# Performance work log

Hardware: AMD Instinct MI355X
Metric: run time of the kernel (lower is better)

Reference implementation:

```python
import jax, jax.numpy as jnp
import numpy as np

B, T, NX, H = 2, 2048, 1024, 16
D = NX // H  # head dim = 64
NEG = -1e9


def setup_inputs() -> dict:
    key = jax.random.key(0)
    ks = jax.random.split(key, 4)
    std = 0.02
    x = jax.random.normal(ks[0], (B, T, NX), dtype=jnp.float32)
    # non-trivial adjacency (lower-triangular) so the masking branch is active
    adj = jnp.tril(jnp.ones((T, T), dtype=jnp.float32))
    w_attn = jax.random.normal(ks[1], (NX, 3 * NX), dtype=jnp.float32) * std
    b_attn = jnp.zeros((3 * NX,), dtype=jnp.float32)
    w_proj = jax.random.normal(ks[2], (NX, NX), dtype=jnp.float32) * std
    b_proj = jnp.zeros((NX,), dtype=jnp.float32)
    w_proj1 = jax.random.normal(ks[3], (NX, NX), dtype=jnp.float32) * std
    b_proj1 = jnp.zeros((NX,), dtype=jnp.float32)
    return {"x": x, "adj": adj, "w_attn": w_attn, "b_attn": b_attn,
            "w_proj": w_proj, "b_proj": b_proj,
            "w_proj1": w_proj1, "b_proj1": b_proj1}


def reference(x, adj, w_attn, b_attn, w_proj, b_proj, w_proj1, b_proj1):
    # c_attn: fused qkv projection  [B,T,3*NX]
    qkv = jnp.einsum('btn,nm->btm', x, w_attn) + b_attn
    q, k, v = jnp.split(qkv, 3, axis=-1)  # each [B,T,NX]

    def heads(t):  # [B,T,NX] -> [B,H,T,D]
        return t.reshape(B, T, H, D).transpose(0, 2, 1, 3)

    qh, kh, vh = heads(q), heads(k), heads(v)
    # scale=False in module default: raw dot-product scores
    w = jnp.einsum('bhqd,bhkd->bhqk', qh, kh)  # [B,H,T,T]
    w = w * adj + NEG * (1.0 - adj)            # custom adjacency mask
    w = jax.nn.softmax(w, axis=-1)
    a = jnp.einsum('bhqk,bhkd->bhqd', w, vh)   # [B,H,T,D]
    a = a.transpose(0, 2, 1, 3).reshape(B, T, NX)  # merge heads
    a = jnp.einsum('btn,nm->btm', a, w_proj) + b_proj
    # residue branch: split+merge of query is identity -> c_proj_1(q)
    re = jnp.einsum('btn,nm->btm', q, w_proj1) + b_proj1
    return a + re
```

## Files before the change

### kernel.cpp

```cpp
#include <hip/hip_runtime.h>
#include <stdint.h>

typedef short s16x8 __attribute__((ext_vector_type(8)));
typedef float f32x4 __attribute__((ext_vector_type(4)));
typedef unsigned int u32x4 __attribute__((ext_vector_type(4)));

#define AS1 __attribute__((address_space(1)))
#define AS3 __attribute__((address_space(3)))

static constexpr int Bc = 2, Tc = 2048, NXc = 1024, Hc = 16;
static constexpr float NEGC = -1e9f;
static constexpr float L2E = 1.44269504088896340736f;
static constexpr float LN2 = 0.69314718055994530942f;

static __device__ __forceinline__ unsigned short f2bf(float f) {
  uint32_t u = __builtin_bit_cast(uint32_t, f);
  u += 0x7fffu + ((u >> 16) & 1u);
  return (unsigned short)(u >> 16);
}

static __device__ __forceinline__ float exp2fast(float x) {
  return __builtin_amdgcn_exp2f(x);
}

static __device__ __forceinline__ uint32_t cvt_pk_bf16(float lo, float hi) {
  uint32_t r;
  asm("v_cvt_pk_bf16_f32 %0, %1, %2" : "=v"(r) : "v"(lo), "v"(hi));
  return r;
}

static __device__ __forceinline__ void gload_lds16(const void* g, void* l) {
  __builtin_amdgcn_global_load_lds((const AS1 uint32_t*)g, (AS3 uint32_t*)l, 16, 0, 0);
}

__global__ __launch_bounds__(256) void k_prep(
    const float* __restrict__ x, unsigned short* __restrict__ xb,
    const float* __restrict__ w_attn, unsigned short* __restrict__ wattnT,
    const float* __restrict__ w_proj, const float* __restrict__ w_proj1,
    unsigned short* __restrict__ wcatT,
    const float* __restrict__ adj, unsigned char* __restrict__ tm) {
  __shared__ float tile[32][33];
  __shared__ int s_any, s_all;
  const int bid = blockIdx.x;
  const int t = threadIdx.x;

  if (bid < 4096) {
    int i = bid * 256 + t;
    float4 v = ((const float4*)x)[i];
    uint32_t lo = (uint32_t)f2bf(v.x) | ((uint32_t)f2bf(v.y) << 16);
    uint32_t hi = (uint32_t)f2bf(v.z) | ((uint32_t)f2bf(v.w) << 16);
    ((uint2*)xb)[i] = make_uint2(lo, hi);
    return;
  }
  if (bid < 9216) {
    const float* src; unsigned short* dst;
    int scols, dld, dkoff, n0, k0; float scale;
    if (bid < 7168) {
      int b = bid - 4096; n0 = (b % 96) * 32; k0 = (b / 96) * 32;
      src = w_attn; scols = 3072; dst = wattnT; dld = 1024; dkoff = 0; scale = 1.0f;
    } else if (bid < 8192) {
      int b = bid - 7168; n0 = (b & 31) * 32; k0 = (b >> 5) * 32;
      src = w_proj; scols = 1024; dst = wcatT; dld = 2048; dkoff = 0; scale = 1.0f;
    } else {
      int b = bid - 8192; n0 = (b & 31) * 32; k0 = (b >> 5) * 32;
      src = w_proj1; scols = 1024; dst = wcatT; dld = 2048; dkoff = 1024; scale = LN2;
    }
    int tx = t & 31, ty = t >> 5;
#pragma unroll
    for (int r = 0; r < 4; r++)
      tile[ty + r * 8][tx] = src[(size_t)(k0 + ty + r * 8) * scols + n0 + tx];
    __syncthreads();
#pragma unroll
    for (int r = 0; r < 4; r++) {
      int n = n0 + ty + r * 8;
      dst[(size_t)n * dld + dkoff + k0 + tx] = f2bf(tile[tx][ty + r * 8] * scale);
    }
    return;
  }
  {
    int b = bid - 9216;
    int kt = b & 31, qt = b >> 5;
    bool anyv = false, all1 = true;
#pragma unroll
    for (int i = 0; i < 4; i++) {
      int e = t * 4 + i;
      int row = e >> 4, c4 = e & 15;
      float4 v = *(const float4*)&adj[(size_t)(qt * 64 + row) * Tc + kt * 64 + c4 * 4];
      anyv |= (v.x != 0.f) | (v.y != 0.f) | (v.z != 0.f) | (v.w != 0.f);
      all1 &= (v.x == 1.f) & (v.y == 1.f) & (v.z == 1.f) & (v.w == 1.f);
    }
    if (t == 0) { s_any = 0; s_all = 1; }
    __syncthreads();
    if (anyv) s_any = 1;
    if (!all1) s_all = 0;
    __syncthreads();
    if (t == 0) tm[qt * 32 + kt] = (unsigned char)(s_any ? (s_all ? 2 : 1) : 0);
  }
}

__global__ __launch_bounds__(256) void k_gemm0(
    const unsigned short* __restrict__ A, int lda,
    const unsigned short* __restrict__ BT, int K,
    const float* __restrict__ bias0, unsigned short* __restrict__ Cb) {
  __shared__ __align__(16) unsigned short As[128 * 32];
  __shared__ __align__(16) unsigned short Bs[128 * 32];
  const int nbx = gridDim.x, nby = gridDim.y;
  const int nwg = nbx * nby;
  int id = blockIdx.y * nbx + blockIdx.x;
  id = (id & 7) * (nwg >> 3) + (id >> 3);
  const int bx = id % nbx;
  const int by = id / nbx;
  const int m0 = by * 128;
  const int n0 = bx * 128;

  const int lane = threadIdx.x & 63;
  const int w = threadIdx.x >> 6;
  const int wr = (w >> 1) * 64;
  const int wc = (w & 1) * 64;
  const int g = lane >> 4, lr = lane & 15;
  const int srow = lane >> 2;
  const int scol = lane & 3;
  f32x4 acc[4][4] = {};

  for (int k0 = 0; k0 < K; k0 += 32) {
    __syncthreads();
#pragma unroll
    for (int i = 0; i < 2; i++) {
      int c = w * 2 + i;
      int row = c * 16 + srow;
      int cs = scol ^ (row & 3);
      gload_lds16(A + (size_t)(m0 + row) * lda + k0 + cs * 8, (void*)(As + c * 512));
      gload_lds16(BT + (size_t)(n0 + row) * K + k0 + cs * 8, (void*)(Bs + c * 512));
    }
    __syncthreads();
    s16x8 af[4], bfr[4];
#pragma unroll
    for (int m = 0; m < 4; m++) {
      int row = wr + m * 16 + lr;
      af[m] = *(const s16x8*)((const char*)As + row * 64 + ((g ^ (row & 3)) * 16));
    }
#pragma unroll
    for (int n = 0; n < 4; n++) {
      int row = wc + n * 16 + lr;
      bfr[n] = *(const s16x8*)((const char*)Bs + row * 64 + ((g ^ (row & 3)) * 16));
    }
#pragma unroll
    for (int m = 0; m < 4; m++)
#pragma unroll
      for (int n = 0; n < 4; n++)
        acc[m][n] = __builtin_amdgcn_mfma_f32_16x16x32_bf16(af[m], bfr[n], acc[m][n], 0, 0, 0);
  }

#pragma unroll
  for (int m = 0; m < 4; m++) {
    int row = m0 + wr + m * 16 + g * 4;
#pragma unroll
    for (int n = 0; n < 4; n++) {
      int col = n0 + wc + n * 16 + lr;
      float bs = bias0[col];
      float sc = (col < NXc) ? L2E : 1.0f;
#pragma unroll
      for (int jj = 0; jj < 4; jj++)
        Cb[(size_t)(row + jj) * 3072 + col] = f2bf((acc[m][n][jj] + bs) * sc);
    }
  }
}

__global__ __launch_bounds__(256) void k_gemm1(
    const unsigned short* __restrict__ A, int lda,
    const unsigned short* __restrict__ A2, int lda2,
    const unsigned short* __restrict__ BT,
    const float* __restrict__ bias0, const float* __restrict__ bias1,
    float* __restrict__ Cf) {
  constexpr int K = 2048, ksplit = 1024;
  __shared__ __align__(16) unsigned short As[2][64 * 32];
  __shared__ __align__(16) unsigned short Bs[2][128 * 32];
  const int nbx = gridDim.x, nby = gridDim.y;
  const int nwg = nbx * nby;
  int id = blockIdx.y * nbx + blockIdx.x;
  id = (id & 7) * (nwg >> 3) + (id >> 3);
  const int bx = id % nbx;
  const int by = id / nbx;
  const int m0 = by * 64;
  const int n0 = bx * 128;

  const int tid = threadIdx.x;
  const int lane = tid & 63;
  const int w = tid >> 6;
  const int wr = (w >> 1) * 32;
  const int wc = (w & 1) * 64;
  const int g = lane >> 4, lr = lane & 15;
  const int srow = lane >> 2;
  const int scol = lane & 3;
  const int arow = tid >> 2;
  f32x4 acc[2][4] = {};

  auto stage = [&](int k0, int buf) {
    {
      int acs = (tid & 3) ^ (arow & 3);
      const unsigned short* ap = (k0 < ksplit)
          ? A + (size_t)(m0 + arow) * lda + k0
          : A2 + (size_t)(m0 + arow) * lda2 + (k0 - ksplit);
      gload_lds16(ap + acs * 8, (void*)(&As[buf][0] + w * 512));
    }
#pragma unroll
    for (int i = 0; i < 2; i++) {
      int c = w * 2 + i;
      int row = c * 16 + srow;
      int cs = scol ^ (row & 3);
      gload_lds16(BT + (size_t)(n0 + row) * K + k0 + cs * 8, (void*)(&Bs[buf][0] + c * 512));
    }
  };

  stage(0, 0);
  __syncthreads();

  for (int k0 = 0; k0 < K; k0 += 32) {
    const int cur = (k0 >> 5) & 1;
    if (k0 + 32 < K) stage(k0 + 32, cur ^ 1);
    s16x8 af[2], bfr[4];
#pragma unroll
    for (int m = 0; m < 2; m++) {
      int row = wr + m * 16 + lr;
      af[m] = *(const s16x8*)((const char*)&As[cur][0] + row * 64 + ((g ^ (row & 3)) * 16));
    }
#pragma unroll
    for (int n = 0; n < 4; n++) {
      int row = wc + n * 16 + lr;
      bfr[n] = *(const s16x8*)((const char*)&Bs[cur][0] + row * 64 + ((g ^ (row & 3)) * 16));
    }
#pragma unroll
    for (int m = 0; m < 2; m++)
#pragma unroll
      for (int n = 0; n < 4; n++)
        acc[m][n] = __builtin_amdgcn_mfma_f32_16x16x32_bf16(af[m], bfr[n], acc[m][n], 0, 0, 0);
    __syncthreads();
  }

#pragma unroll
  for (int m = 0; m < 2; m++) {
    int row = m0 + wr + m * 16 + g * 4;
#pragma unroll
    for (int n = 0; n < 4; n++) {
      int col = n0 + wc + n * 16 + lr;
      float bs = bias0[col] + bias1[col];
#pragma unroll
      for (int jj = 0; jj < 4; jj++)
        Cf[(size_t)(row + jj) * NXc + col] = acc[m][n][jj] + bs;
    }
  }
}

__global__ __launch_bounds__(256) void k_attn(
    const unsigned short* __restrict__ qkv,
    const float* __restrict__ adj,
    const unsigned char* __restrict__ tm,
    unsigned short* __restrict__ acat) {
  __shared__ __align__(16) unsigned short Kb[2][64 * 64];
  __shared__ __align__(16) unsigned short Vt[2][64 * 72];
  __shared__ int s_kts[33];
  __shared__ unsigned char s_tmv[32];
  __shared__ int s_nkt;

  const int bid = blockIdx.x;
  const int qt = 31 - (bid >> 5);
  const int bh = bid & 31;
  const int h = bh & 15;
  const int b = bh >> 4;
  const int q0 = qt * 64;
  const int tid = threadIdx.x;
  const int lane = tid & 63;
  const int w = tid >> 6;
  const int g = lane >> 4, lr = lane & 15;
  const int sc = tid & 7;
  const int sr = tid >> 3;
  const int kvp = 2 * sr;
  const int prp = (kvp & 32) | (((kvp >> 4) & 1) << 2) | ((kvp & 12) << 1) | (kvp & 3);

  if (w == 0) {
    int kt = lane & 31;
    unsigned char v = tm[qt * 32 + kt];
    bool act = (lane < 32) && (v != 0);
    unsigned long long mk = __ballot(act);
    int n = __popcll(mk);
    if (act) {
      int idx = __popcll(mk & ((1ull << lane) - 1));
      s_kts[idx] = kt;
      s_tmv[idx] = v;
      if (idx == n - 1) s_kts[n] = kt;
    }
    if (lane == 0) s_nkt = n;
  }

  s16x8 qf0, qf1;
  {
    size_t base = (size_t)(b * Tc + q0 + w * 16 + lr) * 3072 + h * 64 + g * 8;
    qf0 = *(const s16x8*)(qkv + base);
    qf1 = *(const s16x8*)(qkv + base + 32);
  }
  f32x4 o[4] = {};
  float lrow = 0.f;

  __syncthreads();
  const int nkt = s_nkt;
  if (nkt == 0) return;

  const unsigned short* kbase = qkv + (size_t)(b * Tc) * 3072 + 1024 + h * 64;
  const unsigned short* vbase = kbase + 1024;

  {
    int kt0 = s_kts[0];
    const unsigned short* kb = kbase + (size_t)kt0 * 64 * 3072;
    gload_lds16(kb + (size_t)sr * 3072 + (sc ^ (sr & 7)) * 8, (void*)(&Kb[0][0] + w * 512));
    gload_lds16(kb + (size_t)(sr + 32) * 3072 + (sc ^ (sr & 7)) * 8,
                (void*)(&Kb[0][0] + 2048 + w * 512));
    const unsigned short* vb = vbase + (size_t)kt0 * 64 * 3072;
    s16x8 v0 = *(const s16x8*)(vb + (size_t)kvp * 3072 + sc * 8);
    s16x8 v1 = *(const s16x8*)(vb + (size_t)(kvp + 1) * 3072 + sc * 8);
    char* vt = (char*)&Vt[0][0];
    int pcol = ((prp + sc * 8) & 63) * 2;
#pragma unroll
    for (int j = 0; j < 8; j++) {
      int d = sc * 8 + j;
      uint32_t pk = (uint32_t)(unsigned short)v0[j] |
                    ((uint32_t)(unsigned short)v1[j] << 16);
      *(uint32_t*)(vt + d * 144 + pcol) = pk;
    }
  }
  __syncthreads();

  for (int i = 0; i < nkt; i++) {
    const int cur = i & 1;
    const int kt = s_kts[i];
    const int tmv = s_tmv[i];
    const int kv0 = kt * 64;
    const int nxt = s_kts[i + 1];

    {
      const unsigned short* kb = kbase + (size_t)nxt * 64 * 3072;
      gload_lds16(kb + (size_t)sr * 3072 + (sc ^ (sr & 7)) * 8,
                  (void*)(&Kb[cur ^ 1][0] + w * 512));
      gload_lds16(kb + (size_t)(sr + 32) * 3072 + (sc ^ (sr & 7)) * 8,
                  (void*)(&Kb[cur ^ 1][0] + 2048 + w * 512));
    }
    const unsigned short* vb = vbase + (size_t)nxt * 64 * 3072;
    s16x8 v0 = *(const s16x8*)(vb + (size_t)kvp * 3072 + sc * 8);
    s16x8 v1 = *(const s16x8*)(vb + (size_t)(kvp + 1) * 3072 + sc * 8);

    f32x4 s[4];
    __builtin_amdgcn_s_setprio(1);
#pragma unroll
    for (int n = 0; n < 4; n++) {
      int kvr = n * 16 + lr;
      const char* kr = (const char*)&Kb[cur][0] + kvr * 128;
      s16x8 a0 = *(const s16x8*)(kr + ((g ^ (kvr & 7)) * 16));
      s16x8 a1 = *(const s16x8*)(kr + (((4 + g) ^ (kvr & 7)) * 16));
      f32x4 z = {};
      z = __builtin_amdgcn_mfma_f32_16x16x32_bf16(a0, qf0, z, 0, 0, 0);
      s[n] = __builtin_amdgcn_mfma_f32_16x16x32_bf16(a1, qf1, z, 0, 0, 0);
    }
    __builtin_amdgcn_s_setprio(0);

    if (tmv != 2) {
      const float* arow = adj + (size_t)(q0 + w * 16 + lr) * Tc + kv0;
#pragma unroll
      for (int n = 0; n < 4; n++) {
        float4 a = *(const float4*)(arow + n * 16 + 4 * g);
        s[n][0] = a.x * s[n][0] + NEGC * (1.0f - a.x);
        s[n][1] = a.y * s[n][1] + NEGC * (1.0f - a.y);
        s[n][2] = a.z * s[n][2] + NEGC * (1.0f - a.z);
        s[n][3] = a.w * s[n][3] + NEGC * (1.0f - a.w);
      }
    }

    float ps0 = 0.f, ps1 = 0.f;
#pragma unroll
    for (int n = 0; n < 4; n++) {
      float p0 = exp2fast(s[n][0]), p1 = exp2fast(s[n][1]);
      float p2 = exp2fast(s[n][2]), p3 = exp2fast(s[n][3]);
      s[n][0] = p0; s[n][1] = p1; s[n][2] = p2; s[n][3] = p3;
      ps0 += (p0 + p1); ps1 += (p2 + p3);
    }
    float ps = ps0 + ps1;
    ps += __shfl_xor(ps, 16);
    ps += __shfl_xor(ps, 32);
    lrow += ps;

    u32x4 pw0, pw1;
    pw0.x = cvt_pk_bf16(s[0][0], s[0][1]);
    pw0.y = cvt_pk_bf16(s[0][2], s[0][3]);
    pw0.z = cvt_pk_bf16(s[1][0], s[1][1]);
    pw0.w = cvt_pk_bf16(s[1][2], s[1][3]);
    pw1.x = cvt_pk_bf16(s[2][0], s[2][1]);
    pw1.y = cvt_pk_bf16(s[2][2], s[2][3]);
    pw1.z = cvt_pk_bf16(s[3][0], s[3][1]);
    pw1.w = cvt_pk_bf16(s[3][2], s[3][3]);
    s16x8 pa0 = __builtin_bit_cast(s16x8, pw0);
    s16x8 pa1 = __builtin_bit_cast(s16x8, pw1);

    __builtin_amdgcn_s_setprio(1);
#pragma unroll
    for (int nd = 0; nd < 4; nd++) {
      int d = nd * 16 + lr;
      const char* vrow = (const char*)&Vt[cur][0] + d * 144;
      int swz = (d >> 3) * 8;
      s16x8 vb0 = *(const s16x8*)(vrow + (((8 * g + swz) & 63) * 2));
      s16x8 vb1 = *(const s16x8*)(vrow + (((32 + 8 * g + swz) & 63) * 2));
      o[nd] = __builtin_amdgcn_mfma_f32_16x16x32_bf16(pa0, vb0, o[nd], 0, 0, 0);
      o[nd] = __builtin_amdgcn_mfma_f32_16x16x32_bf16(pa1, vb1, o[nd], 0, 0, 0);
    }
    __builtin_amdgcn_s_setprio(0);

    {
      char* vt = (char*)&Vt[cur ^ 1][0];
      int pcol = ((prp + sc * 8) & 63) * 2;
#pragma unroll
      for (int j = 0; j < 8; j++) {
        int d = sc * 8 + j;
        uint32_t pk = (uint32_t)(unsigned short)v0[j] |
                      ((uint32_t)(unsigned short)v1[j] << 16);
        *(uint32_t*)(vt + d * 144 + pcol) = pk;
      }
    }
    __syncthreads();
  }

  float inv = lrow > 0.f ? 1.0f / lrow : 0.f;
#pragma unroll
  for (int jj = 0; jj < 4; jj++) {
    float iv = __shfl(inv, 4 * g + jj);
    size_t m = (size_t)(b * Tc + q0 + w * 16 + g * 4 + jj);
#pragma unroll
    for (int nd = 0; nd < 4; nd++)
      acat[m * 1024 + h * 64 + nd * 16 + lr] = f2bf(o[nd][jj] * iv);
  }
}

extern "C" void kernel_launch(void* const* d_in, const int* in_sizes, int n_in,
                              void* d_out, int out_size, void* d_ws, size_t ws_size,
                              hipStream_t stream) {
  const float* x       = (const float*)d_in[0];
  const float* adj     = (const float*)d_in[1];
  const float* w_attn  = (const float*)d_in[2];
  const float* b_attn  = (const float*)d_in[3];
  const float* w_proj  = (const float*)d_in[4];
  const float* b_proj  = (const float*)d_in[5];
  const float* w_proj1 = (const float*)d_in[6];
  const float* b_proj1 = (const float*)d_in[7];
  float* out = (float*)d_out;

  char* ws = (char*)d_ws;
  size_t off = 0;
  unsigned short* xb     = (unsigned short*)(ws + off); off += (size_t)4096 * 1024 * 2;
  unsigned short* wattnT = (unsigned short*)(ws + off); off += (size_t)3072 * 1024 * 2;
  unsigned short* wcatT  = (unsigned short*)(ws + off); off += (size_t)1024 * 2048 * 2;
  unsigned short* qkv    = (unsigned short*)(ws + off); off += (size_t)4096 * 3072 * 2;
  unsigned short* acat   = (unsigned short*)(ws + off); off += (size_t)4096 * 1024 * 2;
  unsigned char*  tmask  = (unsigned char*)(ws + off);  off += 1024;
  (void)ws_size; (void)in_sizes; (void)n_in; (void)out_size;

  k_prep<<<10240, 256, 0, stream>>>(x, xb, w_attn, wattnT, w_proj, w_proj1, wcatT,
                                    adj, tmask);
  k_gemm0<<<dim3(24, 32), 256, 0, stream>>>(xb, 1024, wattnT, 1024, b_attn, qkv);
  k_attn<<<1024, 256, 0, stream>>>(qkv, adj, tmask, acat);
  k_gemm1<<<dim3(8, 64), 256, 0, stream>>>(acat, 1024, qkv, 3072,
                                           wcatT, b_proj, b_proj1, out);
}
```

Before: 130.2 us.

## Balance causal attention work by pairing query tiles and splitting KV across blocks

Each attention block now pairs a high query tile with its mirrored low tile. The high tile's KV range is split into two halves: one block handles the first 17 tiles, and the other handles the rest plus the whole low tile. Partial unnormalized outputs and row sums for the upper half of the sequence go to fp32 slabs, and a new combine kernel merges them into acat. The goal is equal work per block so the causal triangle no longer leaves long-tail blocks. The cost is an extra kernel launch and extra fp32 slab traffic.

```diff
diff --git a/kernel.cpp b/kernel.cpp
--- a/kernel.cpp
+++ b/kernel.cpp
@@ -255,19 +255,21 @@
     const unsigned short* __restrict__ qkv,
     const float* __restrict__ adj,
     const unsigned char* __restrict__ tm,
-    unsigned short* __restrict__ acat) {
+    unsigned short* __restrict__ acat,
+    float* __restrict__ o_slab,
+    float* __restrict__ l_slab) {
   __shared__ __align__(16) unsigned short Kb[2][64 * 64];
   __shared__ __align__(16) unsigned short Vt[2][64 * 72];
-  __shared__ int s_kts[33];
-  __shared__ unsigned char s_tmv[32];
-  __shared__ int s_nkt;
+  __shared__ int s_hi[32], s_lo[32];
+  __shared__ int s_nh, s_nl;
 
   const int bid = blockIdx.x;
-  const int qt = 31 - (bid >> 5);
-  const int bh = bid & 31;
+  const int half = bid & 1;
+  const int bh = (bid >> 1) & 31;
+  const int p = bid >> 6;
+  const int qt_hi = 31 - p, qt_lo = p;
   const int h = bh & 15;
   const int b = bh >> 4;
-  const int q0 = qt * 64;
   const int tid = threadIdx.x;
   const int lane = tid & 63;
   const int w = tid >> 6;
@@ -277,7 +279,9 @@
   const int kvp = 2 * sr;
   const int prp = (kvp & 32) | (((kvp >> 4) & 1) << 2) | ((kvp & 12) << 1) | (kvp & 3);
 
-  if (w == 0) {
+  if (w < 2) {
+    int qt = (w == 0) ? qt_hi : qt_lo;
+    int* dst = (w == 0) ? s_hi : s_lo;
     int kt = lane & 31;
     unsigned char v = tm[qt * 32 + kt];
     bool act = (lane < 32) && (v != 0);
@@ -285,134 +289,61 @@
     int n = __popcll(mk);
     if (act) {
       int idx = __popcll(mk & ((1ull << lane) - 1));
-      s_kts[idx] = kt;
-      s_tmv[idx] = v;
-      if (idx == n - 1) s_kts[n] = kt;
-    }
-    if (lane == 0) s_nkt = n;
-  }
+      dst[idx] = kt | ((int)v << 8);
+    }
+    if (lane == 0) { if (w == 0) s_nh = n; else s_nl = n; }
+  }
+  __syncthreads();
+  const int nh = s_nh, nl = s_nl;
+  const int nA = min(nh, 17);
+  const int nhB = nh - nA;
+  const int nit = (half == 0) ? nA : (nhB + nl);
+
+  auto item_at = [&](int i) -> int {
+    if (half == 0) return s_hi[min(i, nA - 1)];
+    if (i < nhB) return s_hi[nA + i];
+    return s_lo[min(i - nhB, nl - 1)];
+  };
+
+  const unsigned short* kbase = qkv + (size_t)(b * Tc) * 3072 + 1024 + h * 64;
+  const unsigned short* vbase = kbase + 1024;
+
+  f32x4 o[4] = {};
+  float lrow = 0.f;
+  bool switched = (half == 1) && (nhB == 0);
+  int cur_q0 = (half == 0 || nhB > 0) ? qt_hi * 64 : qt_lo * 64;
+
+  auto write_partial = [&]() {
+    size_t rbase = (size_t)(half * 2 + b) * 1024 + (qt_hi * 64 - 1024) + w * 16;
+#pragma unroll
+    for (int jj = 0; jj < 4; jj++) {
+      size_t r = rbase + g * 4 + jj;
+#pragma unroll
+      for (int nd = 0; nd < 4; nd++)
+        o_slab[r * 1024 + h * 64 + nd * 16 + lr] = o[nd][jj];
+    }
+    if (g == 0) l_slab[(rbase + lr) * 16 + h] = lrow;
+  };
 
   s16x8 qf0, qf1;
   {
-    size_t base = (size_t)(b * Tc + q0 + w * 16 + lr) * 3072 + h * 64 + g * 8;
+    size_t base = (size_t)(b * Tc + cur_q0 + w * 16 + lr) * 3072 + h * 64 + g * 8;
     qf0 = *(const s16x8*)(qkv + base);
     qf1 = *(const s16x8*)(qkv + base + 32);
   }
-  f32x4 o[4] = {};
-  float lrow = 0.f;
-
-  __syncthreads();
-  const int nkt = s_nkt;
-  if (nkt == 0) return;
-
-  const unsigned short* kbase = qkv + (size_t)(b * Tc) * 3072 + 1024 + h * 64;
-  const unsigned short* vbase = kbase + 1024;
-
-  {
-    int kt0 = s_kts[0];
-    const unsigned short* kb = kbase + (size_t)kt0 * 64 * 3072;
-    gload_lds16(kb + (size_t)sr * 3072 + (sc ^ (sr & 7)) * 8, (void*)(&Kb[0][0] + w * 512));
-    gload_lds16(kb + (size_t)(sr + 32) * 3072 + (sc ^ (sr & 7)) * 8,
-                (void*)(&Kb[0][0] + 2048 + w * 512));
-    const unsigned short* vb = vbase + (size_t)kt0 * 64 * 3072;
-    s16x8 v0 = *(const s16x8*)(vb + (size_t)kvp * 3072 + sc * 8);
-    s16x8 v1 = *(const s16x8*)(vb + (size_t)(kvp + 1) * 3072 + sc * 8);
-    char* vt = (char*)&Vt[0][0];
-    int pcol = ((prp + sc * 8) & 63) * 2;
-#pragma unroll
-    for (int j = 0; j < 8; j++) {
-      int d = sc * 8 + j;
-      uint32_t pk = (uint32_t)(unsigned short)v0[j] |
-                    ((uint32_t)(unsigned short)v1[j] << 16);
-      *(uint32_t*)(vt + d * 144 + pcol) = pk;
-    }
-  }
-  __syncthreads();
-
-  for (int i = 0; i < nkt; i++) {
-    const int cur = i & 1;
-    const int kt = s_kts[i];
-    const int tmv = s_tmv[i];
-    const int kv0 = kt * 64;
-    const int nxt = s_kts[i + 1];
-
+
+  if (nit > 0) {
     {
-      const unsigned short* kb = kbase + (size_t)nxt * 64 * 3072;
-      gload_lds16(kb + (size_t)sr * 3072 + (sc ^ (sr & 7)) * 8,
-                  (void*)(&Kb[cur ^ 1][0] + w * 512));
+      int it0 = item_at(0);
+      int kt0 = it0 & 255;
+      const unsigned short* kb = kbase + (size_t)kt0 * 64 * 3072;
+      gload_lds16(kb + (size_t)sr * 3072 + (sc ^ (sr & 7)) * 8, (void*)(&Kb[0][0] + w * 512));
       gload_lds16(kb + (size_t)(sr + 32) * 3072 + (sc ^ (sr & 7)) * 8,
-                  (void*)(&Kb[cur ^ 1][0] + 2048 + w * 512));
-    }
-    const unsigned short* vb = vbase + (size_t)nxt * 64 * 3072;
-    s16x8 v0 = *(const s16x8*)(vb + (size_t)kvp * 3072 + sc * 8);
-    s16x8 v1 = *(const s16x8*)(vb + (size_t)(kvp + 1) * 3072 + sc * 8);
-
-    f32x4 s[4];
-    __builtin_amdgcn_s_setprio(1);
-#pragma unroll
-    for (int n = 0; n < 4; n++) {
-      int kvr = n * 16 + lr;
-      const char* kr = (const char*)&Kb[cur][0] + kvr * 128;
-      s16x8 a0 = *(const s16x8*)(kr + ((g ^ (kvr & 7)) * 16));
-      s16x8 a1 = *(const s16x8*)(kr + (((4 + g) ^ (kvr & 7)) * 16));
-      f32x4 z = {};
-      z = __builtin_amdgcn_mfma_f32_16x16x32_bf16(a0, qf0, z, 0, 0, 0);
-      s[n] = __builtin_amdgcn_mfma_f32_16x16x32_bf16(a1, qf1, z, 0, 0, 0);
-    }
-    __builtin_amdgcn_s_setprio(0);
-
-    if (tmv != 2) {
-      const float* arow = adj + (size_t)(q0 + w * 16 + lr) * Tc + kv0;
-#pragma unroll
-      for (int n = 0; n < 4; n++) {
-        float4 a = *(const float4*)(arow + n * 16 + 4 * g);
-        s[n][0] = a.x * s[n][0] + NEGC * (1.0f - a.x);
-        s[n][1] = a.y * s[n][1] + NEGC * (1.0f - a.y);
-        s[n][2] = a.z * s[n][2] + NEGC * (1.0f - a.z);
-        s[n][3] = a.w * s[n][3] + NEGC * (1.0f - a.w);
-      }
-    }
-
-    float ps0 = 0.f, ps1 = 0.f;
-#pragma unroll
-    for (int n = 0; n < 4; n++) {
-      float p0 = exp2fast(s[n][0]), p1 = exp2fast(s[n][1]);
-      float p2 = exp2fast(s[n][2]), p3 = exp2fast(s[n][3]);
-      s[n][0] = p0; s[n][1] = p1; s[n][2] = p2; s[n][3] = p3;
-      ps0 += (p0 + p1); ps1 += (p2 + p3);
-    }
-    float ps = ps0 + ps1;
-    ps += __shfl_xor(ps, 16);
-    ps += __shfl_xor(ps, 32);
-    lrow += ps;
-
-    u32x4 pw0, pw1;
-    pw0.x = cvt_pk_bf16(s[0][0], s[0][1]);
-    pw0.y = cvt_pk_bf16(s[0][2], s[0][3]);
-    pw0.z = cvt_pk_bf16(s[1][0], s[1][1]);
-    pw0.w = cvt_pk_bf16(s[1][2], s[1][3]);
-    pw1.x = cvt_pk_bf16(s[2][0], s[2][1]);
-    pw1.y = cvt_pk_bf16(s[2][2], s[2][3]);
-    pw1.z = cvt_pk_bf16(s[3][0], s[3][1]);
-    pw1.w = cvt_pk_bf16(s[3][2], s[3][3]);
-    s16x8 pa0 = __builtin_bit_cast(s16x8, pw0);
-    s16x8 pa1 = __builtin_bit_cast(s16x8, pw1);
-
-    __builtin_amdgcn_s_setprio(1);
-#pragma unroll
-    for (int nd = 0; nd < 4; nd++) {
-      int d = nd * 16 + lr;
-      const char* vrow = (const char*)&Vt[cur][0] + d * 144;
-      int swz = (d >> 3) * 8;
-      s16x8 vb0 = *(const s16x8*)(vrow + (((8 * g + swz) & 63) * 2));
-      s16x8 vb1 = *(const s16x8*)(vrow + (((32 + 8 * g + swz) & 63) * 2));
-      o[nd] = __builtin_amdgcn_mfma_f32_16x16x32_bf16(pa0, vb0, o[nd], 0, 0, 0);
-      o[nd] = __builtin_amdgcn_mfma_f32_16x16x32_bf16(pa1, vb1, o[nd], 0, 0, 0);
-    }
-    __builtin_amdgcn_s_setprio(0);
-
-    {
-      char* vt = (char*)&Vt[cur ^ 1][0];
+                  (void*)(&Kb[0][0] + 2048 + w * 512));
+      const unsigned short* vb = vbase + (size_t)kt0 * 64 * 3072;
+      s16x8 v0 = *(const s16x8*)(vb + (size_t)kvp * 3072 + sc * 8);
+      s16x8 v1 = *(const s16x8*)(vb + (size_t)(kvp + 1) * 3072 + sc * 8);
+      char* vt = (char*)&Vt[0][0];
       int pcol = ((prp + sc * 8) & 63) * 2;
 #pragma unroll
       for (int j = 0; j < 8; j++) {
@@ -423,17 +354,158 @@
       }
     }
     __syncthreads();
-  }
-
+
+    for (int i = 0; i < nit; i++) {
+      if (half == 1 && !switched && i == nhB) {
+        write_partial();
+#pragma unroll
+        for (int nd = 0; nd < 4; nd++) o[nd] = f32x4{0.f, 0.f, 0.f, 0.f};
+        lrow = 0.f;
+        cur_q0 = qt_lo * 64;
+        size_t base = (size_t)(b * Tc + cur_q0 + w * 16 + lr) * 3072 + h * 64 + g * 8;
+        qf0 = *(const s16x8*)(qkv + base);
+        qf1 = *(const s16x8*)(qkv + base + 32);
+        switched = true;
+      }
+      const int cur = i & 1;
+      const int it = item_at(i);
+      const int kt = it & 255;
+      const int tmv = it >> 8;
+      const int kv0 = kt * 64;
+      const int nxt = item_at(min(i + 1, nit - 1)) & 255;
+
+      {
+        const unsigned short* kb = kbase + (size_t)nxt * 64 * 3072;
+        gload_lds16(kb + (size_t)sr * 3072 + (sc ^ (sr & 7)) * 8,
+                    (void*)(&Kb[cur ^ 1][0] + w * 512));
+        gload_lds16(kb + (size_t)(sr + 32) * 3072 + (sc ^ (sr & 7)) * 8,
+                    (void*)(&Kb[cur ^ 1][0] + 2048 + w * 512));
+      }
+      const unsigned short* vb = vbase + (size_t)nxt * 64 * 3072;
+      s16x8 v0 = *(const s16x8*)(vb + (size_t)kvp * 3072 + sc * 8);
+      s16x8 v1 = *(const s16x8*)(vb + (size_t)(kvp + 1) * 3072 + sc * 8);
+
+      f32x4 s[4];
+      __builtin_amdgcn_s_setprio(1);
+#pragma unroll
+      for (int n = 0; n < 4; n++) {
+        int kvr = n * 16 + lr;
+        const char* kr = (const char*)&Kb[cur][0] + kvr * 128;
+        s16x8 a0 = *(const s16x8*)(kr + ((g ^ (kvr & 7)) * 16));
+        s16x8 a1 = *(const s16x8*)(kr + (((4 + g) ^ (kvr & 7)) * 16));
+        f32x4 z = {};
+        z = __builtin_amdgcn_mfma_f32_16x16x32_bf16(a0, qf0, z, 0, 0, 0);
+        s[n] = __builtin_amdgcn_mfma_f32_16x16x32_bf16(a1, qf1, z, 0, 0, 0);
+      }
+      __builtin_amdgcn_s_setprio(0);
+
+      if (tmv != 2) {
+        const float* arow = adj + (size_t)(cur_q0 + w * 16 + lr) * Tc + kv0;
+#pragma unroll
+        for (int n = 0; n < 4; n++) {
+          float4 a = *(const float4*)(arow + n * 16 + 4 * g);
+          s[n][0] = a.x * s[n][0] + NEGC * (1.0f - a.x);
+          s[n][1] = a.y * s[n][1] + NEGC * (1.0f - a.y);
+          s[n][2] = a.z * s[n][2] + NEGC * (1.0f - a.z);
+          s[n][3] = a.w * s[n][3] + NEGC * (1.0f - a.w);
+        }
+      }
+
+      float ps0 = 0.f, ps1 = 0.f;
+#pragma unroll
+      for (int n = 0; n < 4; n++) {
+        float p0 = exp2fast(s[n][0]), p1 = exp2fast(s[n][1]);
+        float p2 = exp2fast(s[n][2]), p3 = exp2fast(s[n][3]);
+        s[n][0] = p0; s[n][1] = p1; s[n][2] = p2; s[n][3] = p3;
+        ps0 += (p0 + p1); ps1 += (p2 + p3);
+      }
+      float ps = ps0 + ps1;
+      ps += __shfl_xor(ps, 16);
+      ps += __shfl_xor(ps, 32);
+      lrow += ps;
+
+      u32x4 pw0, pw1;
+      pw0.x = cvt_pk_bf16(s[0][0], s[0][1]);
+      pw0.y = cvt_pk_bf16(s[0][2], s[0][3]);
+      pw0.z = cvt_pk_bf16(s[1][0], s[1][1]);
+      pw0.w = cvt_pk_bf16(s[1][2], s[1][3]);
+      pw1.x = cvt_pk_bf16(s[2][0], s[2][1]);
+      pw1.y = cvt_pk_bf16(s[2][2], s[2][3]);
+      pw1.z = cvt_pk_bf16(s[3][0], s[3][1]);
+      pw1.w = cvt_pk_bf16(s[3][2], s[3][3]);
+      s16x8 pa0 = __builtin_bit_cast(s16x8, pw0);
+      s16x8 pa1 = __builtin_bit_cast(s16x8, pw1);
+
+      __builtin_amdgcn_s_setprio(1);
+#pragma unroll
+      for (int nd = 0; nd < 4; nd++) {
+        int d = nd * 16 + lr;
+        const char* vrow = (const char*)&Vt[cur][0] + d * 144;
+        int swz = (d >> 3) * 8;
+        s16x8 vb0 = *(const s16x8*)(vrow + (((8 * g + swz) & 63) * 2));
+        s16x8 vb1 = *(const s16x8*)(vrow + (((32 + 8 * g + swz) & 63) * 2));
+        o[nd] = __builtin_amdgcn_mfma_f32_16x16x32_bf16(pa0, vb0, o[nd], 0, 0, 0);
+        o[nd] = __builtin_amdgcn_mfma_f32_16x16x32_bf16(pa1, vb1, o[nd], 0, 0, 0);
+      }
+      __builtin_amdgcn_s_setprio(0);
+
+      {
+        char* vt = (char*)&Vt[cur ^ 1][0];
+        int pcol = ((prp + sc * 8) & 63) * 2;
+#pragma unroll
+        for (int j = 0; j < 8; j++) {
+          int d = sc * 8 + j;
+          uint32_t pk = (uint32_t)(unsigned short)v0[j] |
+                        ((uint32_t)(unsigned short)v1[j] << 16);
+          *(uint32_t*)(vt + d * 144 + pcol) = pk;
+        }
+      }
+      __syncthreads();
+    }
+  }
+
+  if (half == 0) {
+    write_partial();
+    return;
+  }
+  if (!switched) {
+    write_partial();
+#pragma unroll
+    for (int nd = 0; nd < 4; nd++) o[nd] = f32x4{0.f, 0.f, 0.f, 0.f};
+    lrow = 0.f;
+    cur_q0 = qt_lo * 64;
+  }
   float inv = lrow > 0.f ? 1.0f / lrow : 0.f;
 #pragma unroll
   for (int jj = 0; jj < 4; jj++) {
     float iv = __shfl(inv, 4 * g + jj);
-    size_t m = (size_t)(b * Tc + q0 + w * 16 + g * 4 + jj);
+    size_t m = (size_t)(b * Tc + cur_q0 + w * 16 + g * 4 + jj);
 #pragma unroll
     for (int nd = 0; nd < 4; nd++)
       acat[m * 1024 + h * 64 + nd * 16 + lr] = f2bf(o[nd][jj] * iv);
   }
+}
+
+__global__ __launch_bounds__(256) void k_combine(
+    const float* __restrict__ o_slab, const float* __restrict__ l_slab,
+    unsigned short* __restrict__ acat) {
+  int i = blockIdx.x * 256 + threadIdx.x;
+  int c4 = i & 255;
+  int row = (i >> 8) & 1023;
+  int b = i >> 18;
+  size_t i0 = ((size_t)b * 1024 + row) * 256 + c4;
+  size_t i1 = ((size_t)(2 + b) * 1024 + row) * 256 + c4;
+  float4 a = ((const float4*)o_slab)[i0];
+  float4 c = ((const float4*)o_slab)[i1];
+  int h = c4 >> 4;
+  float l0 = l_slab[((size_t)b * 1024 + row) * 16 + h];
+  float l1 = l_slab[((size_t)(2 + b) * 1024 + row) * 16 + h];
+  float ls = l0 + l1;
+  float inv = ls > 0.f ? 1.0f / ls : 0.f;
+  uint2 out;
+  out.x = cvt_pk_bf16((a.x + c.x) * inv, (a.y + c.y) * inv);
+  out.y = cvt_pk_bf16((a.z + c.z) * inv, (a.w + c.w) * inv);
+  ((uint2*)acat)[((size_t)b * 2048 + 1024 + row) * 256 + c4] = out;
 }
 
 extern "C" void kernel_launch(void* const* d_in, const int* in_sizes, int n_in,
@@ -456,13 +528,16 @@
   unsigned short* wcatT  = (unsigned short*)(ws + off); off += (size_t)1024 * 2048 * 2;
   unsigned short* qkv    = (unsigned short*)(ws + off); off += (size_t)4096 * 3072 * 2;
   unsigned short* acat   = (unsigned short*)(ws + off); off += (size_t)4096 * 1024 * 2;
+  float*          o_slab = (float*)(ws + off);          off += (size_t)4 * 1024 * 1024 * 4;
+  float*          l_slab = (float*)(ws + off);          off += (size_t)4 * 1024 * 16 * 4;
   unsigned char*  tmask  = (unsigned char*)(ws + off);  off += 1024;
   (void)ws_size; (void)in_sizes; (void)n_in; (void)out_size;
 
   k_prep<<<10240, 256, 0, stream>>>(x, xb, w_attn, wattnT, w_proj, w_proj1, wcatT,
                                     adj, tmask);
   k_gemm0<<<dim3(24, 32), 256, 0, stream>>>(xb, 1024, wattnT, 1024, b_attn, qkv);
-  k_attn<<<1024, 256, 0, stream>>>(qkv, adj, tmask, acat);
+  k_attn<<<1024, 256, 0, stream>>>(qkv, adj, tmask, acat, o_slab, l_slab);
+  k_combine<<<2048, 256, 0, stream>>>(o_slab, l_slab, acat);
   k_gemm1<<<dim3(8, 64), 256, 0, stream>>>(acat, 1024, qkv, 3072,
                                            wcatT, b_proj, b_proj1, out);
 }
```

Result: slower. 145.3 us (+11.6%).

## Prefetch K/V tiles two steps ahead through registers in attention loop

Applied to the files above, without the earlier changes.

Replaces the direct global-to-LDS K loads with register-staged loads and changes the K/V pipeline so tile i+2 is loaded into registers while tile i+1 is written to LDS at the top of each iteration. This gives global loads a full iteration of compute to hide latency. In exchange it adds VGPR pressure for K registers and routes K through VGPRs instead of async LDS DMA, which may lower occupancy. The s_kts sentinel array grows by one entry so the extra lookahead stays in bounds.

```diff
diff --git a/kernel.cpp b/kernel.cpp
--- a/kernel.cpp
+++ b/kernel.cpp
@@ -258,7 +258,7 @@
     unsigned short* __restrict__ acat) {
   __shared__ __align__(16) unsigned short Kb[2][64 * 64];
   __shared__ __align__(16) unsigned short Vt[2][64 * 72];
-  __shared__ int s_kts[33];
+  __shared__ int s_kts[34];
   __shared__ unsigned char s_tmv[32];
   __shared__ int s_nkt;
 
@@ -287,7 +287,7 @@
       int idx = __popcll(mk & ((1ull << lane) - 1));
       s_kts[idx] = kt;
       s_tmv[idx] = v;
-      if (idx == n - 1) s_kts[n] = kt;
+      if (idx == n - 1) { s_kts[n] = kt; s_kts[n + 1] = kt; }
     }
     if (lane == 0) s_nkt = n;
   }
@@ -308,25 +308,39 @@
   const unsigned short* kbase = qkv + (size_t)(b * Tc) * 3072 + 1024 + h * 64;
   const unsigned short* vbase = kbase + 1024;
 
-  {
-    int kt0 = s_kts[0];
-    const unsigned short* kb = kbase + (size_t)kt0 * 64 * 3072;
-    gload_lds16(kb + (size_t)sr * 3072 + (sc ^ (sr & 7)) * 8, (void*)(&Kb[0][0] + w * 512));
-    gload_lds16(kb + (size_t)(sr + 32) * 3072 + (sc ^ (sr & 7)) * 8,
-                (void*)(&Kb[0][0] + 2048 + w * 512));
-    const unsigned short* vb = vbase + (size_t)kt0 * 64 * 3072;
-    s16x8 v0 = *(const s16x8*)(vb + (size_t)kvp * 3072 + sc * 8);
-    s16x8 v1 = *(const s16x8*)(vb + (size_t)(kvp + 1) * 3072 + sc * 8);
-    char* vt = (char*)&Vt[0][0];
-    int pcol = ((prp + sc * 8) & 63) * 2;
+  const size_t koff0 = (size_t)sr * 3072 + (sc ^ (sr & 7)) * 8;
+  const size_t koff1 = (size_t)(sr + 32) * 3072 + (sc ^ (sr & 7)) * 8;
+  const int kd0 = w * 1024 + lane * 16;
+  const int kd1 = kd0 + 4096;
+  const size_t voff0 = (size_t)kvp * 3072 + sc * 8;
+  const size_t voff1 = (size_t)(kvp + 1) * 3072 + sc * 8;
+  const int pcol = ((prp + sc * 8) & 63) * 2;
+
+  s16x8 kA0, kA1, vA0, vA1;
+  auto load_tile = [&](int kt) {
+    const unsigned short* kb = kbase + (size_t)kt * 64 * 3072;
+    const unsigned short* vb = vbase + (size_t)kt * 64 * 3072;
+    kA0 = *(const s16x8*)(kb + koff0);
+    kA1 = *(const s16x8*)(kb + koff1);
+    vA0 = *(const s16x8*)(vb + voff0);
+    vA1 = *(const s16x8*)(vb + voff1);
+  };
+  auto write_tile = [&](int buf) {
+    *(s16x8*)((char*)&Kb[buf][0] + kd0) = kA0;
+    *(s16x8*)((char*)&Kb[buf][0] + kd1) = kA1;
+    char* vt = (char*)&Vt[buf][0];
 #pragma unroll
     for (int j = 0; j < 8; j++) {
       int d = sc * 8 + j;
-      uint32_t pk = (uint32_t)(unsigned short)v0[j] |
-                    ((uint32_t)(unsigned short)v1[j] << 16);
+      uint32_t pk = (uint32_t)(unsigned short)vA0[j] |
+                    ((uint32_t)(unsigned short)vA1[j] << 16);
       *(uint32_t*)(vt + d * 144 + pcol) = pk;
     }
-  }
+  };
+
+  load_tile(s_kts[0]);
+  write_tile(0);
+  load_tile(s_kts[1]);
   __syncthreads();
 
   for (int i = 0; i < nkt; i++) {
@@ -334,18 +348,9 @@
     const int kt = s_kts[i];
     const int tmv = s_tmv[i];
     const int kv0 = kt * 64;
-    const int nxt = s_kts[i + 1];
-
-    {
-      const unsigned short* kb = kbase + (size_t)nxt * 64 * 3072;
-      gload_lds16(kb + (size_t)sr * 3072 + (sc ^ (sr & 7)) * 8,
-                  (void*)(&Kb[cur ^ 1][0] + w * 512));
-      gload_lds16(kb + (size_t)(sr + 32) * 3072 + (sc ^ (sr & 7)) * 8,
-                  (void*)(&Kb[cur ^ 1][0] + 2048 + w * 512));
-    }
-    const unsigned short* vb = vbase + (size_t)nxt * 64 * 3072;
-    s16x8 v0 = *(const s16x8*)(vb + (size_t)kvp * 3072 + sc * 8);
-    s16x8 v1 = *(const s16x8*)(vb + (size_t)(kvp + 1) * 3072 + sc * 8);
+
+    write_tile(cur ^ 1);
+    load_tile(s_kts[i + 2]);
 
     f32x4 s[4];
     __builtin_amdgcn_s_setprio(1);
@@ -411,17 +416,6 @@
     }
     __builtin_amdgcn_s_setprio(0);
 
-    {
-      char* vt = (char*)&Vt[cur ^ 1][0];
-      int pcol = ((prp + sc * 8) & 63) * 2;
-#pragma unroll
-      for (int j = 0; j < 8; j++) {
-        int d = sc * 8 + j;
-        uint32_t pk = (uint32_t)(unsigned short)v0[j] |
-                      ((uint32_t)(unsigned short)v1[j] << 16);
-        *(uint32_t*)(vt + d * 144 + pcol) = pk;
-      }
-    }
     __syncthreads();
   }
 
```

After: 125.2 us. 3.9% less time.
